# Kernel optimization log

Measured on AMD Instinct MI355X. Metric: run time of the kernel, lower is better.

The kernel has to match this reference:

```python
import jax, jax.numpy as jnp
import numpy as np

EPS = 1e-5

def _bn(z, g, b):
    # train-mode BatchNorm2d: batch stats over (B,H,W), biased variance
    mean = z.mean(axis=(0, 2, 3), keepdims=True)
    var = z.var(axis=(0, 2, 3), keepdims=True)
    return g[None, :, None, None] * (z - mean) * jax.lax.rsqrt(var + EPS) + b[None, :, None, None]

def _conv1x1(x, w):
    # x: [B,C,H,W], w: [O,C] -> [B,O,H,W]
    return jnp.einsum('bchw,oc->bohw', x, w)

def _proj(x, w1, g1, b1, w2, g2, b2):
    z = _bn(_conv1x1(x, w1), g1, b1)
    return _bn(_conv1x1(z, w2), g2, b2)

def setup_inputs() -> dict:
    key = jax.random.key(0)
    ks = jax.random.split(key, 24)
    B, Cx, Cy, M, H, W = 4, 512, 256, 64, 64, 64
    f32 = jnp.float32
    def wmat(k, o, c):
        return jax.random.normal(k, (o, c), f32) * (c ** -0.5)
    def gamma(k, c):
        return 1.0 + 0.1 * jax.random.normal(k, (c,), f32)
    def beta(k, c):
        return 0.1 * jax.random.normal(k, (c,), f32)
    inp = {
        'x': jax.random.normal(ks[0], (B, Cx, H, W), f32),
        'y': jax.random.normal(ks[1], (B, Cy, H, W), f32),
        # f_self
        'ws1': wmat(ks[2], M, Cx), 'gs1': gamma(ks[3], M), 'bs1': beta(ks[4], M),
        'ws2': wmat(ks[5], M, M),  'gs2': gamma(ks[6], M), 'bs2': beta(ks[7], M),
        # f_x
        'wx1': wmat(ks[8], M, Cx), 'gx1': gamma(ks[9], M), 'bx1': beta(ks[10], M),
        'wx2': wmat(ks[11], M, M), 'gx2': gamma(ks[12], M), 'bx2': beta(ks[13], M),
        # f_y
        'wy1': wmat(ks[14], M, Cy), 'gy1': gamma(ks[15], M), 'by1': beta(ks[16], M),
        'wy2': wmat(ks[17], M, M),  'gy2': gamma(ks[18], M), 'by2': beta(ks[19], M),
        # f_up
        'wu': wmat(ks[20], Cx, M), 'gu': gamma(ks[21], Cx), 'bu': beta(ks[22], Cx),
    }
    return inp

def reference(x, y, ws1, gs1, bs1, ws2, gs2, bs2,
              wx1, gx1, bx1, wx2, gx2, bx2,
              wy1, gy1, by1, wy2, gy2, by2,
              wu, gu, bu):
    B, C, H, W = x.shape
    M = ws1.shape[0]
    N = H * W
    fself = _proj(x, ws1, gs1, bs1, ws2, gs2, bs2).reshape(B, M, N).transpose(0, 2, 1)  # [B,N,M]
    fx = _proj(x, wx1, gx1, bx1, wx2, gx2, bx2).reshape(B, M, N).transpose(0, 2, 1)      # [B,N,M]
    fy = _proj(y, wy1, gy1, by1, wy2, gy2, by2).reshape(B, M, N)                          # [B,M,N]
    sim = jnp.matmul(fx, fy)                  # [B,N,N]  (scale=False)
    attn = jax.nn.softmax(sim, axis=-1)
    fout = jnp.matmul(attn, fself)            # [B,N,M]
    fout = fout.transpose(0, 2, 1).reshape(B, M, H, W)
    out = _bn(_conv1x1(fout, wu), gu, bu)
    return x + out
```

## Files before the change

### kernel.cpp

```cpp
#include <hip/hip_runtime.h>
#include <hip/hip_fp16.h>
#include <cstdint>

constexpr int N_ = 4096;
constexpr float CNT = 16384.f;

typedef __attribute__((ext_vector_type(8))) _Float16 half8;
typedef __attribute__((ext_vector_type(4))) float f32x4;
union fragh { half8 h8; int i4[4]; };

__device__ inline int pkh(float a, float b) {
  union { __half2 h; int i; } u;
  u.h = __float22half2_rn(float2{a, b});
  return u.i;
}
__device__ inline void pk_hl(float a, float b, int& h, int& l) {
  __half ah = __float2half_rn(a), bh = __float2half_rn(b);
  union { __half2 v; int i; } u;
  u.v = __halves2half2(ah, bh);
  h = u.i;
  float ar = a - __half2float(ah), br = b - __half2float(bh);
  union { __half2 v; int i; } w2;
  w2.v = __float22half2_rn(float2{ar, br});
  l = w2.i;
}
__device__ inline float2 uph(int v) {
  union { __half2 h; int i; } u;
  u.i = v;
  return float2{__half2float(__low2half(u.h)), __half2float(__high2half(u.h))};
}


__global__ __launch_bounds__(256) void packA_k(const float* __restrict__ x,
                                               const float* __restrict__ y,
                                               int* __restrict__ Afx,
                                               int* __restrict__ Afy) {
  const int job = blockIdx.y;
  if (job == 1 && blockIdx.x >= 2048) return;
  const int idx = blockIdx.x * 256 + threadIdx.x;
  const float* src = job ? y : x;
  int* dst = job ? Afy : Afx;
  const int KT = job ? 8 : 16;
  const int loOff = job ? 2097152 : 4194304;
  const int n = idx & 4095, q = (idx >> 12) & 3;
  const int kt = job ? ((idx >> 14) & 7) : ((idx >> 14) & 15);
  const int b = job ? (idx >> 17) : (idx >> 18);
  const float* sp = src + ((size_t)(b * (KT * 32) + kt * 32 + q * 8)) * N_ + n;
  float a[8];
#pragma unroll
  for (int j = 0; j < 8; ++j) a[j] = sp[(size_t)j * N_];
  int4 hi, lo;
  pk_hl(a[0], a[1], hi.x, lo.x);
  pk_hl(a[2], a[3], hi.y, lo.y);
  pk_hl(a[4], a[5], hi.z, lo.z);
  pk_hl(a[6], a[7], hi.w, lo.w);
  const int base = (((b * KT + kt) * 256 + (n >> 4)) * 64 + q * 16 + (n & 15)) * 4;
  *(int4*)&dst[base] = hi;
  *(int4*)&dst[loOff + base] = lo;
}

__global__ __launch_bounds__(256) void prep1_k(const float* __restrict__ ws1,
                                               const float* __restrict__ wx1,
                                               const float* __restrict__ wy1,
                                               int* __restrict__ wt1f) {
  const int idx = blockIdx.x * 256 + threadIdx.x;
  const float* W;
  int KT, K, hiBase, loOff, e;
  if (idx < 16384) { W = ws1; KT = 16; K = 512; hiBase = 0; loOff = 16384; e = idx; }
  else if (idx < 32768) { W = wx1; KT = 16; K = 512; hiBase = 32768; loOff = 16384; e = idx - 16384; }
  else { W = wy1; KT = 8; K = 256; hiBase = 65536; loOff = 8192; e = idx - 32768; }
  const int jj = e & 3, lane = (e >> 2) & 63;
  int kt, ot;
  if (KT == 16) { kt = (e >> 8) & 15; ot = e >> 12; } else { kt = (e >> 8) & 7; ot = e >> 11; }
  const int o = ot * 16 + (lane & 15);
  const int k = kt * 32 + (lane >> 4) * 8 + 2 * jj;
  int h, l;
  pk_hl(W[o * K + k], W[o * K + k + 1], h, l);
  wt1f[hiBase + e] = h;
  wt1f[hiBase + loOff + e] = l;
}

__global__ __launch_bounds__(256) void prep2_k(
    const float* __restrict__ ws2, const float* __restrict__ wx2,
    const float* __restrict__ wy2,
    const float* __restrict__ gs1, const float* __restrict__ bs1,
    const float* __restrict__ gx1, const float* __restrict__ bx1,
    const float* __restrict__ gy1, const float* __restrict__ by1,
    const float* __restrict__ stats, int* __restrict__ wt2f,
    float* __restrict__ biasf) {
  const int branch = blockIdx.x;
  const int t = threadIdx.x;
  const float* W = branch == 0 ? ws2 : (branch == 1 ? wx2 : wy2);
  const float* g1 = branch == 0 ? gs1 : (branch == 1 ? gx1 : gy1);
  const float* b1 = branch == 0 ? bs1 : (branch == 1 ? bx1 : by1);
  const float* stin = stats + branch * 128;
  int* outW = wt2f + branch * 4096;

  auto scale = [&](int k) {
    float mean = stin[k] * (1.f / CNT);
    float var = stin[64 + k] * (1.f / CNT) - mean * mean;
    return g1[k] * rsqrtf(var + 1e-5f);
  };
#pragma unroll
  for (int i = 0; i < 8; ++i) {
    int e = i * 256 + t;
    int jj = e & 3, lane = (e >> 2) & 63, kt = (e >> 8) & 1, ot = e >> 9;
    int o = ot * 16 + (lane & 15);
    int k = kt * 32 + (lane >> 4) * 8 + 2 * jj;
    float w0 = W[o * 64 + k] * scale(k);
    float w1 = W[o * 64 + k + 1] * scale(k + 1);
    int h, l;
    pk_hl(w0, w1, h, l);
    outW[e] = h;
    outW[2048 + e] = l;
  }
  if (t < 64) {
    float s = 0.f;
    for (int k = 0; k < 64; ++k) {
      float mean = stin[k] * (1.f / CNT);
      float var = stin[64 + k] * (1.f / CNT) - mean * mean;
      float sc = g1[k] * rsqrtf(var + 1e-5f);
      float sh = b1[k] - mean * sc;
      s += W[t * 64 + k] * sh;
    }
    biasf[branch * 64 + t] = s;
  }
}

__global__ __launch_bounds__(256) void prepu_k(const float* __restrict__ wu,
                                               float* __restrict__ wut) {
  int e = blockIdx.x * 256 + threadIdx.x;
  int k = e >> 9, o = e & 511;
  wut[e] = wu[o * 64 + k];
}

__global__ __launch_bounds__(64) void conv1_k(
    const int* __restrict__ Afx, const int* __restrict__ Afy,
    const int* __restrict__ wt1f, int* __restrict__ z1f,
    float* __restrict__ stats) {
  const int lane = threadIdx.x;
  const int la = lane & 15;
  const int quad = lane >> 4;
  const int b = blockIdx.x >> 6;
  const int ns = blockIdx.x & 63;
  const int branch = blockIdx.y;
  const int KT = branch == 2 ? 8 : 16;
  const int* Af = branch == 2 ? Afy : Afx;
  const int aLo = branch == 2 ? 2097152 : 4194304;
  const int* Wf = wt1f + (branch == 0 ? 0 : (branch == 1 ? 32768 : 65536));
  const int wLo = branch == 2 ? 8192 : 16384;
  float* st = stats + branch * 128;
  int* zb = z1f + branch * 1048576;
  const int ntg0 = ns * 4;

  f32x4 acc[4][4];
#pragma unroll
  for (int i = 0; i < 4; ++i)
#pragma unroll
    for (int j = 0; j < 4; ++j) acc[i][j] = f32x4{0.f, 0.f, 0.f, 0.f};

  auto loadF = [&](int kt, fragh (&wh)[4], fragh (&wl)[4], fragh (&ah)[4],
                   fragh (&al)[4]) {
#pragma unroll
    for (int ot = 0; ot < 4; ++ot) {
      const int base = ((ot * KT + kt) * 64 + lane) * 4;
      *(int4*)wh[ot].i4 = *(const int4*)&Wf[base];
      *(int4*)wl[ot].i4 = *(const int4*)&Wf[wLo + base];
    }
#pragma unroll
    for (int nt = 0; nt < 4; ++nt) {
      const int abase = (((b * KT + kt) * 256 + ntg0 + nt) * 64 + lane) * 4;
      *(int4*)ah[nt].i4 = *(const int4*)&Af[abase];
      *(int4*)al[nt].i4 = *(const int4*)&Af[aLo + abase];
    }
  };
  auto mm = [&](fragh (&wh)[4], fragh (&wl)[4], fragh (&ah)[4], fragh (&al)[4]) {
#pragma unroll
    for (int ot = 0; ot < 4; ++ot)
#pragma unroll
      for (int nt = 0; nt < 4; ++nt) {
        acc[ot][nt] = __builtin_amdgcn_mfma_f32_16x16x32_f16(wh[ot].h8, ah[nt].h8, acc[ot][nt], 0, 0, 0);
        acc[ot][nt] = __builtin_amdgcn_mfma_f32_16x16x32_f16(wh[ot].h8, al[nt].h8, acc[ot][nt], 0, 0, 0);
        acc[ot][nt] = __builtin_amdgcn_mfma_f32_16x16x32_f16(wl[ot].h8, ah[nt].h8, acc[ot][nt], 0, 0, 0);
      }
  };

  fragh whA[4], wlA[4], ahA[4], alA[4];
  fragh whB[4], wlB[4], ahB[4], alB[4];
  loadF(0, whA, wlA, ahA, alA);
#pragma unroll 1
  for (int kt = 0; kt < KT; kt += 2) {
    loadF(kt + 1, whB, wlB, ahB, alB);
    mm(whA, wlA, ahA, alA);
    const int k2 = (kt + 2 < KT) ? kt + 2 : kt;
    loadF(k2, whA, wlA, ahA, alA);
    mm(whB, wlB, ahB, alB);
  }

#pragma unroll
  for (int ot = 0; ot < 4; ++ot) {
    const int ktz = ot >> 1;
    const int qz = (ot & 1) * 2 + (quad >> 1);
    const int jz = (quad & 1) * 2;
#pragma unroll
    for (int nt = 0; nt < 4; ++nt) {
      const int addr = (((b * 2 + ktz) * 256 + ntg0 + nt) * 64 + qz * 16 + la) * 4 + jz;
      int h0, l0, h1, l1;
      pk_hl(acc[ot][nt][0], acc[ot][nt][1], h0, l0);
      pk_hl(acc[ot][nt][2], acc[ot][nt][3], h1, l1);
      *(int2*)&zb[addr] = int2{h0, h1};
      *(int2*)&zb[524288 + addr] = int2{l0, l1};
    }
  }
#pragma unroll
  for (int ot = 0; ot < 4; ++ot)
#pragma unroll
    for (int r = 0; r < 4; ++r) {
      float s = acc[ot][0][r] + acc[ot][1][r] + acc[ot][2][r] + acc[ot][3][r];
      float q = acc[ot][0][r] * acc[ot][0][r] + acc[ot][1][r] * acc[ot][1][r] +
                acc[ot][2][r] * acc[ot][2][r] + acc[ot][3][r] * acc[ot][3][r];
#pragma unroll
      for (int d = 1; d < 16; d <<= 1) { s += __shfl_xor(s, d); q += __shfl_xor(q, d); }
      if (la == 0) {
        atomicAdd(&st[ot * 16 + quad * 4 + r], s);
        atomicAdd(&st[64 + ot * 16 + quad * 4 + r], q);
      }
    }
}

__global__ __launch_bounds__(64) void conv2_k(
    const int* __restrict__ z1f, const int* __restrict__ wt2f,
    const float* __restrict__ biasf, int* __restrict__ z2f,
    float* __restrict__ stats) {
  const int lane = threadIdx.x;
  const int la = lane & 15;
  const int quad = lane >> 4;
  const int b = blockIdx.x >> 6;
  const int ns = blockIdx.x & 63;
  const int branch = blockIdx.y;
  const int* Af = z1f + branch * 1048576;
  const int* Wf = wt2f + branch * 4096;
  const float* bias = biasf + branch * 64;
  float* st = stats + (3 + branch) * 128;
  int* zb = z2f + branch * 1048576;
  const int ntg0 = ns * 4;

  f32x4 acc[4][4];
#pragma unroll
  for (int ot = 0; ot < 4; ++ot)
#pragma unroll
    for (int nt = 0; nt < 4; ++nt) {
#pragma unroll
      for (int r = 0; r < 4; ++r) acc[ot][nt][r] = bias[ot * 16 + quad * 4 + r];
    }

  auto loadF = [&](int kt, fragh (&wh)[4], fragh (&wl)[4], fragh (&ah)[4],
                   fragh (&al)[4]) {
#pragma unroll
    for (int ot = 0; ot < 4; ++ot) {
      const int base = ((ot * 2 + kt) * 64 + lane) * 4;
      *(int4*)wh[ot].i4 = *(const int4*)&Wf[base];
      *(int4*)wl[ot].i4 = *(const int4*)&Wf[2048 + base];
    }
#pragma unroll
    for (int nt = 0; nt < 4; ++nt) {
      const int abase = (((b * 2 + kt) * 256 + ntg0 + nt) * 64 + lane) * 4;
      *(int4*)ah[nt].i4 = *(const int4*)&Af[abase];
      *(int4*)al[nt].i4 = *(const int4*)&Af[524288 + abase];
    }
  };
  auto mm = [&](fragh (&wh)[4], fragh (&wl)[4], fragh (&ah)[4], fragh (&al)[4]) {
#pragma unroll
    for (int ot = 0; ot < 4; ++ot)
#pragma unroll
      for (int nt = 0; nt < 4; ++nt) {
        acc[ot][nt] = __builtin_amdgcn_mfma_f32_16x16x32_f16(wh[ot].h8, ah[nt].h8, acc[ot][nt], 0, 0, 0);
        acc[ot][nt] = __builtin_amdgcn_mfma_f32_16x16x32_f16(wh[ot].h8, al[nt].h8, acc[ot][nt], 0, 0, 0);
        acc[ot][nt] = __builtin_amdgcn_mfma_f32_16x16x32_f16(wl[ot].h8, ah[nt].h8, acc[ot][nt], 0, 0, 0);
      }
  };

  fragh whA[4], wlA[4], ahA[4], alA[4];
  fragh whB[4], wlB[4], ahB[4], alB[4];
  loadF(0, whA, wlA, ahA, alA);
  loadF(1, whB, wlB, ahB, alB);
  mm(whA, wlA, ahA, alA);
  mm(whB, wlB, ahB, alB);

#pragma unroll
  for (int ot = 0; ot < 4; ++ot) {
    const int ktz = ot >> 1;
    const int qz = (ot & 1) * 2 + (quad >> 1);
    const int jz = (quad & 1) * 2;
#pragma unroll
    for (int nt = 0; nt < 4; ++nt) {
      const int addr = (((b * 2 + ktz) * 256 + ntg0 + nt) * 64 + qz * 16 + la) * 4 + jz;
      int h0, l0, h1, l1;
      pk_hl(acc[ot][nt][0], acc[ot][nt][1], h0, l0);
      pk_hl(acc[ot][nt][2], acc[ot][nt][3], h1, l1);
      *(int2*)&zb[addr] = int2{h0, h1};
      *(int2*)&zb[524288 + addr] = int2{l0, l1};
    }
  }
#pragma unroll
  for (int ot = 0; ot < 4; ++ot)
#pragma unroll
    for (int r = 0; r < 4; ++r) {
      float s = acc[ot][0][r] + acc[ot][1][r] + acc[ot][2][r] + acc[ot][3][r];
      float q = acc[ot][0][r] * acc[ot][0][r] + acc[ot][1][r] * acc[ot][1][r] +
                acc[ot][2][r] * acc[ot][2][r] + acc[ot][3][r] * acc[ot][3][r];
#pragma unroll
      for (int d = 1; d < 16; d <<= 1) { s += __shfl_xor(s, d); q += __shfl_xor(q, d); }
      if (la == 0) {
        atomicAdd(&st[ot * 16 + quad * 4 + r], s);
        atomicAdd(&st[64 + ot * 16 + quad * 4 + r], q);
      }
    }
}

__global__ __launch_bounds__(256) void pack_k(
    const int* __restrict__ z2f,
    const float* __restrict__ gs2, const float* __restrict__ bs2,
    const float* __restrict__ gx2, const float* __restrict__ bx2,
    const float* __restrict__ gy2, const float* __restrict__ by2,
    int* __restrict__ Qf, int* __restrict__ Kf, int* __restrict__ Vf,
    const float* __restrict__ stats) {
  const int job = blockIdx.z;
  const int idx = blockIdx.x * 256 + threadIdx.x;
  const float* g2 = job == 0 ? gx2 : (job == 1 ? gy2 : gs2);
  const float* b2 = job == 0 ? bx2 : (job == 1 ? by2 : bs2);
  const float* st = stats + (job == 0 ? 4 : (job == 1 ? 5 : 3)) * 128;

  auto snorm = [&](int c, float& s, float& h) {
    float mean = st[c] * (1.f / CNT);
    float var = st[64 + c] * (1.f / CNT) - mean * mean;
    float r = rsqrtf(var + 1e-5f);
    s = g2[c] * r;
    h = b2[c] - mean * s;
  };
  if (job < 2) {
    const int* zf = z2f + (job == 0 ? 1048576 : 2097152);
    int* outp = job == 0 ? Qf : Kf;
    int h = zf[idx], l = zf[524288 + idx];
    int jj = idx & 3, lane = (idx >> 2) & 63, q = lane >> 4;
    int kt = (idx >> 16) & 1;
    int c0 = 2 * (kt * 16 + q * 4 + jj);
    float s0, h0, s1, h1;
    snorm(c0, s0, h0);
    snorm(c0 + 1, s1, h1);
    float2 vh = uph(h), vl = uph(l);
    outp[idx] = pkh((vh.x + vl.x) * s0 + h0, (vh.y + vl.y) * s1 + h1);
  } else {
    int w_ = idx & 3, lane = (idx >> 2) & 63, la_v = lane & 15, q_v = lane >> 4;
    int mt = (idx >> 8) & 3, kb = (idx >> 10) & 127, b = idx >> 17;
    int ch = mt * 16 + la_v;
    int k = kb * 16 + q_v * 4 + w_;
    int n0 = 2 * k;
    int kp = ch >> 1, kt = kp >> 4, qz = (kp >> 2) & 3, jz = kp & 3, half = ch & 1;
    int a0 = (((b * 2 + kt) * 256 + (n0 >> 4)) * 64 + qz * 16 + (n0 & 15)) * 4 + jz;
    float2 h0v = uph(z2f[a0]), l0v = uph(z2f[524288 + a0]);
    float2 h1v = uph(z2f[a0 + 4]), l1v = uph(z2f[524288 + a0 + 4]);
    float v0 = half ? (h0v.y + l0v.y) : (h0v.x + l0v.x);
    float v1 = half ? (h1v.y + l1v.y) : (h1v.x + l1v.x);
    float s0, h0;
    snorm(ch, s0, h0);
    Vf[idx] = pkh(v0 * s0 + h0, v1 * s0 + h0);
  }
}

__global__ __launch_bounds__(256, 4) void attn_k(const int* __restrict__ Qf,
                                                 const int* __restrict__ Kf,
                                                 const int* __restrict__ Vf,
                                                 float* __restrict__ fout) {
  const int tid = threadIdx.x;
  const int lane = tid & 63;
  const int wid = tid >> 6;
  const int la = lane & 15;
  const int quad = lane >> 4;
  const int b = blockIdx.x & 3;
  const int qbase = (blockIdx.x >> 2) * 16;
  const int* Qb = Qf + (size_t)b * 131072;
  const int* Kb4 = Kf + (size_t)b * 131072;
  const int* Vb4 = Vf + (size_t)b * 131072;

  __shared__ union USm {
    int P16[4][16 * 20];
    struct { float O[4][16][69]; float M[4][16]; float L[4][16]; } e;
  } smu;
  int* myP = smu.P16[wid];

  fragh aq[2];
#pragma unroll
  for (int c = 0; c < 2; ++c)
    *(int4*)aq[c].i4 =
        *(const int4*)&Qb[((c * 256 + (qbase >> 4)) * 64 + quad * 16 + la) * 4];

  f32x4 o[4];
  float mrun = -3.0e38f, lrun = 0.f;
#pragma unroll
  for (int mt = 0; mt < 4; ++mt) o[mt] = f32x4{0.f, 0.f, 0.f, 0.f};

  const int jbeg = wid * (N_ / 4);
  const int jend = jbeg + N_ / 4;

  int4 ka[2][2], kb2[2][2];
#pragma unroll
  for (int nt = 0; nt < 2; ++nt)
#pragma unroll
    for (int g = 0; g < 2; ++g)
      ka[nt][g] = *(const int4*)&Kb4[((g * 256 + (jbeg >> 4) + nt) * 64 + lane) * 4];

  auto body = [&](int j0, int4 (&kc)[2][2], int4 (&kn)[2][2]) {
    f32x4 s[2];
#pragma unroll
    for (int nt = 0; nt < 2; ++nt) {
      fragh k0, k1;
      k0.i4[0] = kc[nt][0].x; k0.i4[1] = kc[nt][0].y;
      k0.i4[2] = kc[nt][0].z; k0.i4[3] = kc[nt][0].w;
      k1.i4[0] = kc[nt][1].x; k1.i4[1] = kc[nt][1].y;
      k1.i4[2] = kc[nt][1].z; k1.i4[3] = kc[nt][1].w;
      f32x4 z = f32x4{0.f, 0.f, 0.f, 0.f};
      z = __builtin_amdgcn_mfma_f32_16x16x32_f16(k0.h8, aq[0].h8, z, 0, 0, 0);
      s[nt] = __builtin_amdgcn_mfma_f32_16x16x32_f16(k1.h8, aq[1].h8, z, 0, 0, 0);
    }
    int4 vv[4];
#pragma unroll
    for (int mt = 0; mt < 4; ++mt)
      vv[mt] = *(const int4*)&Vb4[(((j0 >> 5) * 4 + mt) * 64 + lane) * 4];
    const int nj = (j0 + 32 < jend) ? (j0 + 32) : jbeg;
#pragma unroll
    for (int nt = 0; nt < 2; ++nt)
#pragma unroll
      for (int g = 0; g < 2; ++g)
        kn[nt][g] = *(const int4*)&Kb4[((g * 256 + (nj >> 4) + nt) * 64 + lane) * 4];
    float t0 = fmaxf(fmaxf(s[0][0], s[0][1]), fmaxf(s[0][2], s[0][3]));
    float t1 = fmaxf(fmaxf(s[1][0], s[1][1]), fmaxf(s[1][2], s[1][3]));
    float t = fmaxf(t0, t1);
    t = fmaxf(t, __shfl_xor(t, 16));
    t = fmaxf(t, __shfl_xor(t, 32));
    float mnew = fmaxf(mrun, t);
    float alpha = __expf(mrun - mnew);
    float p[2][4];
    float ps = 0.f;
#pragma unroll
    for (int nt = 0; nt < 2; ++nt)
#pragma unroll
      for (int r = 0; r < 4; ++r) {
        p[nt][r] = __expf(s[nt][r] - mnew);
        ps += p[nt][r];
      }
    ps += __shfl_xor(ps, 16);
    ps += __shfl_xor(ps, 32);
    lrun = lrun * alpha + ps;
    mrun = mnew;
#pragma unroll
    for (int nt = 0; nt < 2; ++nt) {
      myP[(nt * 8 + quad * 2 + 0) * 20 + la] = pkh(p[nt][0], p[nt][1]);
      myP[(nt * 8 + quad * 2 + 1) * 20 + la] = pkh(p[nt][2], p[nt][3]);
    }
    __asm__ __volatile__("s_waitcnt lgkmcnt(0)" ::: "memory");
    fragh pb;
#pragma unroll
    for (int j = 0; j < 4; ++j) pb.i4[j] = myP[(quad * 4 + j) * 20 + la];
#pragma unroll
    for (int mt = 0; mt < 4; ++mt) {
      o[mt][0] *= alpha; o[mt][1] *= alpha;
      o[mt][2] *= alpha; o[mt][3] *= alpha;
    }
#pragma unroll
    for (int mt = 0; mt < 4; ++mt) {
      fragh vb;
      vb.i4[0] = vv[mt].x; vb.i4[1] = vv[mt].y;
      vb.i4[2] = vv[mt].z; vb.i4[3] = vv[mt].w;
      o[mt] = __builtin_amdgcn_mfma_f32_16x16x32_f16(vb.h8, pb.h8, o[mt], 0, 0, 0);
    }
  };

#pragma unroll 1
  for (int j0 = jbeg; j0 < jend; j0 += 64) {
    body(j0, ka, kb2);
    body(j0 + 32, kb2, ka);
  }

  __syncthreads();
  if (quad == 0) {
    smu.e.M[wid][la] = mrun;
    smu.e.L[wid][la] = lrun;
  }
#pragma unroll
  for (int mt = 0; mt < 4; ++mt)
#pragma unroll
    for (int r = 0; r < 4; ++r) smu.e.O[wid][la][mt * 16 + quad * 4 + r] = o[mt][r];
  __syncthreads();

#pragma unroll
  for (int t = 0; t < 4; ++t) {
    int oidx = t * 256 + tid;
    int m = oidx >> 4;
    int q = oidx & 15;
    float m0 = fmaxf(fmaxf(smu.e.M[0][q], smu.e.M[1][q]),
                     fmaxf(smu.e.M[2][q], smu.e.M[3][q]));
    float num = 0.f, den = 0.f;
#pragma unroll
    for (int w = 0; w < 4; ++w) {
      float wgt = __expf(smu.e.M[w][q] - m0);
      num += wgt * smu.e.O[w][q][m];
      den += wgt * smu.e.L[w][q];
    }
    fout[((size_t)b * 64 + m) * N_ + qbase + q] = num / den;
  }
}

__global__ __launch_bounds__(256) void convup_k(const float* __restrict__ fout,
                                                const float* __restrict__ wut,
                                                float* __restrict__ u,
                                                float* __restrict__ stats) {
  const int t = threadIdx.x;
  const int b = blockIdx.x >> 4;
  const int n0 = (blockIdx.x & 15) * 256;
  const int o0 = blockIdx.y * 64;

  __shared__ float sA[16][260];
  __shared__ float sW[16][68];

  const int ng4 = (t & 31) * 4;
  const int og8 = (t >> 5) * 8;
  float acc[8][8];
#pragma unroll
  for (int i = 0; i < 8; ++i)
#pragma unroll
    for (int j = 0; j < 8; ++j) acc[i][j] = 0.f;

  const float* Ap = fout + ((size_t)b * 64 + (t >> 6)) * N_ + n0 + (t & 63) * 4;
  const float* Wp = wut + (size_t)(t >> 4) * 512 + o0 + (t & 15) * 4;
  const int arow = t >> 6, acol = (t & 63) * 4;
  const int wrow = t >> 4, wcol = (t & 15) * 4;

  float4 pa[4];
  float4 pw;
#pragma unroll
  for (int i = 0; i < 4; ++i) pa[i] = *(const float4*)(Ap + (size_t)(4 * i) * N_);
  pw = *(const float4*)Wp;
  Ap += (size_t)16 * N_;
  Wp += 16 * 512;
#pragma unroll
  for (int i = 0; i < 4; ++i) *(float4*)&sA[arow + 4 * i][acol] = pa[i];
  *(float4*)&sW[wrow][wcol] = pw;
  __syncthreads();

#pragma unroll 1
  for (int k0 = 0; k0 < 64; k0 += 16) {
    const bool more = (k0 + 16) < 64;
    if (more) {
#pragma unroll
      for (int i = 0; i < 4; ++i) pa[i] = *(const float4*)(Ap + (size_t)(4 * i) * N_);
      pw = *(const float4*)Wp;
      Ap += (size_t)16 * N_;
      Wp += 16 * 512;
    }
#pragma unroll
    for (int k = 0; k < 16; ++k) {
      float4 a0 = *(const float4*)&sA[k][ng4];
      float4 a1 = *(const float4*)&sA[k][128 + ng4];
      float4 w0 = *(const float4*)&sW[k][og8];
      float4 w1 = *(const float4*)&sW[k][og8 + 4];
      float av[8] = {a0.x, a0.y, a0.z, a0.w, a1.x, a1.y, a1.z, a1.w};
      float wv[8] = {w0.x, w0.y, w0.z, w0.w, w1.x, w1.y, w1.z, w1.w};
#pragma unroll
      for (int i = 0; i < 8; ++i)
#pragma unroll
        for (int j = 0; j < 8; ++j) acc[i][j] = fmaf(wv[i], av[j], acc[i][j]);
    }
    __syncthreads();
    if (more) {
#pragma unroll
      for (int i = 0; i < 4; ++i) *(float4*)&sA[arow + 4 * i][acol] = pa[i];
      *(float4*)&sW[wrow][wcol] = pw;
    }
    __syncthreads();
  }

  float* Cb = u + ((size_t)b * 512 + o0 + og8) * N_ + n0;
#pragma unroll
  for (int i = 0; i < 8; ++i) {
    float4 v0 = {acc[i][0], acc[i][1], acc[i][2], acc[i][3]};
    float4 v1 = {acc[i][4], acc[i][5], acc[i][6], acc[i][7]};
    *(float4*)&Cb[(size_t)i * N_ + ng4] = v0;
    *(float4*)&Cb[(size_t)i * N_ + 128 + ng4] = v1;
  }
#pragma unroll
  for (int i = 0; i < 8; ++i) {
    float s = 0.f, q = 0.f;
#pragma unroll
    for (int j = 0; j < 8; ++j) { s += acc[i][j]; q += acc[i][j] * acc[i][j]; }
#pragma unroll
    for (int d = 1; d < 32; d <<= 1) { s += __shfl_xor(s, d); q += __shfl_xor(q, d); }
    if ((t & 31) == 0) {
      atomicAdd(&stats[768 + o0 + og8 + i], s);
      atomicAdd(&stats[1280 + o0 + og8 + i], q);
    }
  }
}

__global__ __launch_bounds__(256) void final_k(const float* __restrict__ x,
                                               const float* __restrict__ u,
                                               const float* __restrict__ gu,
                                               const float* __restrict__ bu,
                                               const float* __restrict__ stats,
                                               float* __restrict__ out) {
  size_t idx = (size_t)blockIdx.x * 256 + threadIdx.x;
  int c = (int)((idx >> 12) & 511);
  float mean = stats[768 + c] * (1.f / CNT);
  float var = stats[1280 + c] * (1.f / CNT) - mean * mean;
  float r = rsqrtf(var + 1e-5f);
  float s = gu[c] * r;
  float sh = bu[c] - mean * s;
  out[idx] = x[idx] + u[idx] * s + sh;
}

extern "C" void kernel_launch(void* const* d_in, const int* in_sizes, int n_in,
                              void* d_out, int out_size, void* d_ws, size_t ws_size,
                              hipStream_t stream) {
  const float* x = (const float*)d_in[0];
  const float* y = (const float*)d_in[1];
  const float* ws1 = (const float*)d_in[2];
  const float* gs1 = (const float*)d_in[3];
  const float* bs1 = (const float*)d_in[4];
  const float* ws2 = (const float*)d_in[5];
  const float* gs2 = (const float*)d_in[6];
  const float* bs2 = (const float*)d_in[7];
  const float* wx1 = (const float*)d_in[8];
  const float* gx1 = (const float*)d_in[9];
  const float* bx1 = (const float*)d_in[10];
  const float* wx2 = (const float*)d_in[11];
  const float* gx2 = (const float*)d_in[12];
  const float* bx2 = (const float*)d_in[13];
  const float* wy1 = (const float*)d_in[14];
  const float* gy1 = (const float*)d_in[15];
  const float* by1 = (const float*)d_in[16];
  const float* wy2 = (const float*)d_in[17];
  const float* gy2 = (const float*)d_in[18];
  const float* by2 = (const float*)d_in[19];
  const float* wu = (const float*)d_in[20];
  const float* gu = (const float*)d_in[21];
  const float* bu = (const float*)d_in[22];
  float* out = (float*)d_out;

  float* w = (float*)d_ws;
  const size_t M1 = 1048576;
  int* z1f = (int*)w;
  int* z2f = (int*)(w + 3 * M1);
  float* fout = w + 6 * M1;
  float* u = w + 7 * M1;
  int* Afx = (int*)u;
  int* Afy = (int*)(w + 3 * M1);
  int* Qf = (int*)(w + 15 * M1);
  int* Kf = Qf + 524288;
  int* Vf = Kf + 524288;
  float* stats = (float*)(Vf + 524288);
  int* wt1f = (int*)(stats + 1792);
  int* wt2f = wt1f + 81920;
  float* biasf = (float*)(wt2f + 12288);
  float* wut = biasf + 192;

  hipMemsetAsync(stats, 0, 1792 * sizeof(float), stream);

  prep1_k<<<dim3(160), dim3(256), 0, stream>>>(ws1, wx1, wy1, wt1f);
  packA_k<<<dim3(4096, 2), dim3(256), 0, stream>>>(x, y, Afx, Afy);
  conv1_k<<<dim3(256, 3), dim3(64), 0, stream>>>(Afx, Afy, wt1f, z1f, stats);
  prep2_k<<<dim3(3), dim3(256), 0, stream>>>(ws2, wx2, wy2, gs1, bs1, gx1, bx1,
                                             gy1, by1, stats, wt2f, biasf);
  conv2_k<<<dim3(256, 3), dim3(64), 0, stream>>>(z1f, wt2f, biasf, z2f, stats);
  prepu_k<<<dim3(128), dim3(256), 0, stream>>>(wu, wut);
  pack_k<<<dim3(2048, 1, 3), dim3(256), 0, stream>>>(z2f, gs2, bs2, gx2, bx2, gy2,
                                                     by2, Qf, Kf, Vf, stats);
  attn_k<<<dim3(1024), dim3(256), 0, stream>>>(Qf, Kf, Vf, fout);
  convup_k<<<dim3(64, 8), dim3(256), 0, stream>>>(fout, wut, u, stats);
  final_k<<<dim3(32768), dim3(256), 0, stream>>>(x, u, gu, bu, stats, out);
}
```

Before: 367.8 us.

## Stage conv1 operands through LDS with async global_load_lds and two waves

conv1_k now launches two waves per block instead of one. Wave 0 loads the weight fragments and wave 1 loads the activation fragments into a double-buffered LDS tile using global_load_lds. Each wave then computes half of the column tiles, reading weights from LDS, so weight fetches are shared instead of duplicated per wave. This cuts register pressure and global load traffic, but adds a __syncthreads per K step and relies on the implicit wait semantics of the async LDS loads.

```diff
diff --git a/kernel.cpp b/kernel.cpp
--- a/kernel.cpp
+++ b/kernel.cpp
@@ -28,6 +28,12 @@
   union { __half2 h; int i; } u;
   u.i = v;
   return float2{__half2float(__low2half(u.h)), __half2float(__high2half(u.h))};
+}
+
+__device__ inline void gll(const int* g, int* l) {
+  __builtin_amdgcn_global_load_lds(
+      (const __attribute__((address_space(1))) void*)g,
+      (__attribute__((address_space(3))) void*)l, 16, 0, 0);
 }
 
 
@@ -134,11 +140,13 @@
   wut[e] = wu[o * 64 + k];
 }
 
-__global__ __launch_bounds__(64) void conv1_k(
+__global__ __launch_bounds__(128) void conv1_k(
     const int* __restrict__ Afx, const int* __restrict__ Afy,
     const int* __restrict__ wt1f, int* __restrict__ z1f,
     float* __restrict__ stats) {
-  const int lane = threadIdx.x;
+  const int t = threadIdx.x;
+  const int lane = t & 63;
+  const int wv = t >> 6;
   const int la = lane & 15;
   const int quad = lane >> 4;
   const int b = blockIdx.x >> 6;
@@ -153,48 +161,61 @@
   int* zb = z1f + branch * 1048576;
   const int ntg0 = ns * 4;
 
-  f32x4 acc[4][4];
-#pragma unroll
-  for (int i = 0; i < 4; ++i)
-#pragma unroll
-    for (int j = 0; j < 4; ++j) acc[i][j] = f32x4{0.f, 0.f, 0.f, 0.f};
-
-  auto loadF = [&](int kt, fragh (&wh)[4], fragh (&wl)[4], fragh (&ah)[4],
-                   fragh (&al)[4]) {
+  __shared__ int lds[2][16][256];
+
+  f32x4 acc[4][2];
+#pragma unroll
+  for (int ot = 0; ot < 4; ++ot)
+#pragma unroll
+    for (int nt = 0; nt < 2; ++nt) acc[ot][nt] = f32x4{0.f, 0.f, 0.f, 0.f};
+
+  auto stage = [&](int buf, int kt) {
+    if (wv == 0) {
+#pragma unroll
+      for (int ot = 0; ot < 4; ++ot) {
+        const int cb = (ot * KT + kt) * 256;
+        gll(Wf + cb + lane * 4, &lds[buf][ot][0]);
+        gll(Wf + wLo + cb + lane * 4, &lds[buf][4 + ot][0]);
+      }
+    } else {
+#pragma unroll
+      for (int nt = 0; nt < 4; ++nt) {
+        const int ab = ((b * KT + kt) * 256 + ntg0 + nt) * 256;
+        gll(Af + ab + lane * 4, &lds[buf][8 + nt][0]);
+        gll(Af + aLo + ab + lane * 4, &lds[buf][12 + nt][0]);
+      }
+    }
+  };
+  auto compute = [&](int buf) {
+    fragh wh[4], wl[4], ah[2], al[2];
 #pragma unroll
     for (int ot = 0; ot < 4; ++ot) {
-      const int base = ((ot * KT + kt) * 64 + lane) * 4;
-      *(int4*)wh[ot].i4 = *(const int4*)&Wf[base];
-      *(int4*)wl[ot].i4 = *(const int4*)&Wf[wLo + base];
-    }
-#pragma unroll
-    for (int nt = 0; nt < 4; ++nt) {
-      const int abase = (((b * KT + kt) * 256 + ntg0 + nt) * 64 + lane) * 4;
-      *(int4*)ah[nt].i4 = *(const int4*)&Af[abase];
-      *(int4*)al[nt].i4 = *(const int4*)&Af[aLo + abase];
-    }
-  };
-  auto mm = [&](fragh (&wh)[4], fragh (&wl)[4], fragh (&ah)[4], fragh (&al)[4]) {
+      *(int4*)wh[ot].i4 = *(const int4*)&lds[buf][ot][lane * 4];
+      *(int4*)wl[ot].i4 = *(const int4*)&lds[buf][4 + ot][lane * 4];
+    }
+#pragma unroll
+    for (int nt = 0; nt < 2; ++nt) {
+      *(int4*)ah[nt].i4 = *(const int4*)&lds[buf][8 + wv * 2 + nt][lane * 4];
+      *(int4*)al[nt].i4 = *(const int4*)&lds[buf][12 + wv * 2 + nt][lane * 4];
+    }
 #pragma unroll
     for (int ot = 0; ot < 4; ++ot)
 #pragma unroll
-      for (int nt = 0; nt < 4; ++nt) {
+      for (int nt = 0; nt < 2; ++nt) {
         acc[ot][nt] = __builtin_amdgcn_mfma_f32_16x16x32_f16(wh[ot].h8, ah[nt].h8, acc[ot][nt], 0, 0, 0);
         acc[ot][nt] = __builtin_amdgcn_mfma_f32_16x16x32_f16(wh[ot].h8, al[nt].h8, acc[ot][nt], 0, 0, 0);
         acc[ot][nt] = __builtin_amdgcn_mfma_f32_16x16x32_f16(wl[ot].h8, ah[nt].h8, acc[ot][nt], 0, 0, 0);
       }
   };
 
-  fragh whA[4], wlA[4], ahA[4], alA[4];
-  fragh whB[4], wlB[4], ahB[4], alB[4];
-  loadF(0, whA, wlA, ahA, alA);
+  stage(0, 0);
+  int cur = 0;
 #pragma unroll 1
-  for (int kt = 0; kt < KT; kt += 2) {
-    loadF(kt + 1, whB, wlB, ahB, alB);
-    mm(whA, wlA, ahA, alA);
-    const int k2 = (kt + 2 < KT) ? kt + 2 : kt;
-    loadF(k2, whA, wlA, ahA, alA);
-    mm(whB, wlB, ahB, alB);
+  for (int kt = 0; kt < KT; ++kt) {
+    __syncthreads();
+    if (kt + 1 < KT) stage(cur ^ 1, kt + 1);
+    compute(cur);
+    cur ^= 1;
   }
 
 #pragma unroll
@@ -203,8 +224,9 @@
     const int qz = (ot & 1) * 2 + (quad >> 1);
     const int jz = (quad & 1) * 2;
 #pragma unroll
-    for (int nt = 0; nt < 4; ++nt) {
-      const int addr = (((b * 2 + ktz) * 256 + ntg0 + nt) * 64 + qz * 16 + la) * 4 + jz;
+    for (int nt = 0; nt < 2; ++nt) {
+      const int addr =
+          (((b * 2 + ktz) * 256 + ntg0 + wv * 2 + nt) * 64 + qz * 16 + la) * 4 + jz;
       int h0, l0, h1, l1;
       pk_hl(acc[ot][nt][0], acc[ot][nt][1], h0, l0);
       pk_hl(acc[ot][nt][2], acc[ot][nt][3], h1, l1);
@@ -216,9 +238,8 @@
   for (int ot = 0; ot < 4; ++ot)
 #pragma unroll
     for (int r = 0; r < 4; ++r) {
-      float s = acc[ot][0][r] + acc[ot][1][r] + acc[ot][2][r] + acc[ot][3][r];
-      float q = acc[ot][0][r] * acc[ot][0][r] + acc[ot][1][r] * acc[ot][1][r] +
-                acc[ot][2][r] * acc[ot][2][r] + acc[ot][3][r] * acc[ot][3][r];
+      float s = acc[ot][0][r] + acc[ot][1][r];
+      float q = acc[ot][0][r] * acc[ot][0][r] + acc[ot][1][r] * acc[ot][1][r];
 #pragma unroll
       for (int d = 1; d < 16; d <<= 1) { s += __shfl_xor(s, d); q += __shfl_xor(q, d); }
       if (la == 0) {
@@ -667,7 +688,7 @@
 
   prep1_k<<<dim3(160), dim3(256), 0, stream>>>(ws1, wx1, wy1, wt1f);
   packA_k<<<dim3(4096, 2), dim3(256), 0, stream>>>(x, y, Afx, Afy);
-  conv1_k<<<dim3(256, 3), dim3(64), 0, stream>>>(Afx, Afy, wt1f, z1f, stats);
+  conv1_k<<<dim3(256, 3), dim3(128), 0, stream>>>(Afx, Afy, wt1f, z1f, stats);
   prep2_k<<<dim3(3), dim3(256), 0, stream>>>(ws2, wx2, wy2, gs1, bs1, gx1, bx1,
                                              gy1, by1, stats, wt2f, biasf);
   conv2_k<<<dim3(256, 3), dim3(64), 0, stream>>>(z1f, wt2f, biasf, z2f, stats);
```

After: 389.1 us. 5.8% more time.
